# Performance work log

Measured on AMD Instinct MI355X. Metric: run time of the kernel, lower is better.

Reference implementation:

```python
import jax, jax.numpy as jnp
import numpy as np

B, T, E, H, L, Q, FF, V, C = 4, 2048, 16, 4, 2, 16, 64, 32000, 16
D = E // H  # head_dim = 4


def pos_encoding(t, e):
    # Sinusoidal PE, matching torch: pe[:,0::2]=sin, pe[:,1::2]=cos
    pos = jnp.arange(t, dtype=jnp.float32)[:, None]
    div = jnp.exp(jnp.arange(0, e, 2, dtype=jnp.float32) * (-np.log(10000.0) / e))
    ang = pos * div  # [T, E/2]
    return jnp.stack([jnp.sin(ang), jnp.cos(ang)], axis=-1).reshape(t, e)


def setup_inputs() -> dict:
    key = jax.random.key(0)
    ks = jax.random.split(key, 12)
    def n(k, shape, scale=0.1):
        return (jax.random.normal(k, shape) * scale).astype(jnp.float32)
    return {
        "tokens": jax.random.randint(ks[0], (B, T), 0, V),
        "emb": n(ks[1], (V, E)),
        "Wq": n(ks[2], (L, E, E)), "Wk": n(ks[3], (L, E, E)),
        "Wv": n(ks[4], (L, E, E)), "Wo": n(ks[5], (L, E, E)),
        "theta": n(ks[6], (L, Q), 1.0),
        "W1": n(ks[7], (L, E, FF)), "b1": jnp.zeros((L, FF), jnp.float32),
        "W2": n(ks[8], (L, FF, E)), "b2": jnp.zeros((L, E), jnp.float32),
        "gamma": jnp.ones((E,), jnp.float32), "beta": jnp.zeros((E,), jnp.float32),
        "Wc": n(ks[9], (E, C)), "bc": jnp.zeros((C,), jnp.float32),
    }


def reference(tokens, emb, Wq, Wk, Wv, Wo, theta, W1, b1, W2, b2, gamma, beta, Wc, bc):
    x = emb[tokens] + pos_encoding(T, E)[None]  # [B,T,E]
    for l in range(L):  # fixed small layer count
        # --- multi-head self-attention (no mask, eval mode: dropout off) ---
        q = (x @ Wq[l]).reshape(B, T, H, D)
        k = (x @ Wk[l]).reshape(B, T, H, D)
        v = (x @ Wv[l]).reshape(B, T, H, D)
        scores = jnp.einsum('bqhd,bkhd->bhqk', q, k) / np.sqrt(D).astype(np.float32)
        attn = jax.nn.softmax(scores, axis=-1)  # [B,H,T,T]
        o = jnp.einsum('bhqk,bkhd->bqhd', attn, v).reshape(B, T, E) @ Wo[l]
        x = x + o
        # --- quantum feed-forward ---
        # RX(x_w)|0> then RY(theta_w), measure PauliZ per wire. Single-qubit
        # gates on a product state factorize exactly: <Z_w> = cos(theta_w)*cos(x_w)
        q_out = jnp.cos(theta[l]) * jnp.cos(x)  # [B,T,E]
        h = jax.nn.relu(q_out @ W1[l] + b1[l])
        x = x + (h @ W2[l] + b2[l])
    # final LayerNorm
    mu = x.mean(-1, keepdims=True)
    var = ((x - mu) ** 2).mean(-1, keepdims=True)
    x = (x - mu) / jnp.sqrt(var + 1e-5) * gamma + beta
    # mean pool over tokens + classifier
    return x.mean(axis=1) @ Wc + bc  # [B,C]
```

## Files before the change

### kernel.cpp

```cpp
#include <hip/hip_runtime.h>
#include <hip/hip_bf16.h>
#include <math.h>

#define B_ 4
#define T_ 2048
#define E_ 16
#define H_ 4
#define D_ 4
#define L_ 2
#define FF_ 64
#define C_ 16

#define QSCALE 0.7213475204444817f

typedef __hip_bfloat16 bf16;
typedef _Float16 h8 __attribute__((ext_vector_type(8)));
typedef float f4 __attribute__((ext_vector_type(4)));

#if __has_builtin(__builtin_amdgcn_exp2f)
__device__ __forceinline__ float fast_exp2(float x) { return __builtin_amdgcn_exp2f(x); }
#else
__device__ __forceinline__ float fast_exp2(float x) { return exp2f(x); }
#endif

__device__ __forceinline__ unsigned short f2h(float f) {
  _Float16 h = (_Float16)f;
  return __builtin_bit_cast(unsigned short, h);
}
__device__ __forceinline__ _Float16 h2(unsigned short u) {
  return __builtin_bit_cast(_Float16, u);
}

__device__ __forceinline__ bool probe_bf16(const void* gamma) {
  return ((const unsigned*)gamma)[0] == 0x3F803F80u;
}
__device__ __forceinline__ float ldin(const void* p, int i, bool isb) {
  if (isb) {
    unsigned short u = ((const unsigned short*)p)[i];
    union { unsigned x; float f; } c; c.x = ((unsigned)u) << 16;
    return c.f;
  }
  return ((const float*)p)[i];
}
__device__ __forceinline__ void unpack2(unsigned u, float& a, float& b) {
  union { unsigned x; float f; } lo, hi;
  lo.x = u << 16; hi.x = u & 0xffff0000u;
  a = lo.f; b = hi.f;
}

__global__ __launch_bounds__(64) void embed_qkv_kernel(
    const int* __restrict__ tokens, const void* __restrict__ emb,
    const void* __restrict__ Wq, const void* __restrict__ Wk, const void* __restrict__ Wv,
    int wofs, const void* __restrict__ gamma,
    float* __restrict__ X, ushort4* __restrict__ Qhp, ushort4* __restrict__ Khp,
    float4* __restrict__ Vfp) {
  __shared__ float wq[256], wk[256], wv[256];
  bool isb = probe_bf16(gamma);
  int tid = threadIdx.x;
  #pragma unroll
  for (int i = tid; i < 256; i += 64) {
    wq[i] = ldin(Wq, wofs + i, isb);
    wk[i] = ldin(Wk, wofs + i, isb);
    wv[i] = ldin(Wv, wofs + i, isb);
  }
  int r = tid & 31, half = tid >> 5;
  int row = blockIdx.x * 32 + r;
  int t = row & (T_ - 1);
  int tok = tokens[row];
  float x[16];
  if (isb) {
    const unsigned short* eb = (const unsigned short*)emb + (size_t)tok * E_;
    uint4 e0 = ((const uint4*)eb)[0], e1 = ((const uint4*)eb)[1];
    unpack2(e0.x, x[0], x[1]);   unpack2(e0.y, x[2], x[3]);
    unpack2(e0.z, x[4], x[5]);   unpack2(e0.w, x[6], x[7]);
    unpack2(e1.x, x[8], x[9]);   unpack2(e1.y, x[10], x[11]);
    unpack2(e1.z, x[12], x[13]); unpack2(e1.w, x[14], x[15]);
  } else {
    const float* er = (const float*)emb + (size_t)tok * E_;
    #pragma unroll
    for (int i = 0; i < 4; i++) {
      float4 f = ((const float4*)er)[i];
      x[4*i+0] = f.x; x[4*i+1] = f.y; x[4*i+2] = f.z; x[4*i+3] = f.w;
    }
  }
  const float divs[8] = {1.f, 0.31622776601683794f, 0.1f, 0.031622776601683794f,
                         0.01f, 0.0031622776601683794f, 0.001f, 0.00031622776601683794f};
  #pragma unroll
  for (int i = 0; i < 8; i++) {
    float ang = (float)t * divs[i];
    x[2*i]   += __sinf(ang);
    x[2*i+1] += __cosf(ang);
  }
  __syncthreads();
  if (half == 0) {
    float* xr = X + (size_t)row * E_;
    #pragma unroll
    for (int i = 0; i < 4; i++)
      ((float4*)xr)[i] = make_float4(x[4*i], x[4*i+1], x[4*i+2], x[4*i+3]);
  }
  int b = row >> 11;
  #pragma unroll
  for (int hh = 0; hh < 2; hh++) {
    int h = half * 2 + hh;
    float q[4] = {0,0,0,0}, k[4] = {0,0,0,0}, v[4] = {0,0,0,0};
    #pragma unroll
    for (int e = 0; e < 16; e++) {
      float xv = x[e];
      #pragma unroll
      for (int d = 0; d < 4; d++) {
        q[d] = fmaf(xv, wq[e*16 + h*4 + d], q[d]);
        k[d] = fmaf(xv, wk[e*16 + h*4 + d], k[d]);
        v[d] = fmaf(xv, wv[e*16 + h*4 + d], v[d]);
      }
    }
    size_t idx = (size_t)(b * H_ + h) * T_ + t;
    Qhp[idx] = make_ushort4(f2h(q[0]*QSCALE), f2h(q[1]*QSCALE),
                            f2h(q[2]*QSCALE), f2h(q[3]*QSCALE));
    Khp[idx] = make_ushort4(f2h(k[0]), f2h(k[1]), f2h(k[2]), f2h(k[3]));
    Vfp[idx] = make_float4(v[0], v[1], v[2], v[3]);
  }
}

__global__ __launch_bounds__(256) void attn_kernel(
    const ushort4* __restrict__ Qhp, const ushort4* __restrict__ Khp,
    const float4* __restrict__ Vfp, float* __restrict__ Ob) {
  __shared__ float part[2][2][4][20];
  int blk = blockIdx.x;
  int bh = blk >> 6;
  int qp = blk & 63;
  int tid = threadIdx.x;
  int lane = tid & 63;
  int w = tid >> 6;
  int qt_l = w >> 1;
  int ks = w & 1;
  int qbase = qp * 32 + qt_l * 16;
  int kl = lane & 15;
  size_t bhT = (size_t)bh * T_;
  const _Float16 z = (_Float16)0.f;
  ushort4 qv = make_ushort4(0, 0, 0, 0);
  if (lane < 16) qv = Qhp[bhT + qbase + lane];
  h8 afrag = {h2(qv.x), h2(qv.y), h2(qv.z), h2(qv.w), z, z, z, z};
  f4 zero4 = {0.f, 0.f, 0.f, 0.f};
  float o[4][4] = {{0,0,0,0},{0,0,0,0},{0,0,0,0},{0,0,0,0}};
  float lr[4] = {0,0,0,0};
  int kt0 = ks * 64;
  #pragma unroll 4
  for (int kt = kt0; kt < kt0 + 64; kt++) {
    ushort4 kv = Khp[bhT + kt*16 + kl];
    if (lane >= 16) kv = make_ushort4(0, 0, 0, 0);
    h8 bfrag = {h2(kv.x), h2(kv.y), h2(kv.z), h2(kv.w), z, z, z, z};
    f4 sc = __builtin_amdgcn_mfma_f32_16x16x32_f16(afrag, bfrag, zero4, 0, 0, 0);
    float4 v = Vfp[bhT + kt*16 + kl];
    float p0 = fast_exp2(sc[0]), p1 = fast_exp2(sc[1]);
    float p2 = fast_exp2(sc[2]), p3 = fast_exp2(sc[3]);
    lr[0] += p0; lr[1] += p1; lr[2] += p2; lr[3] += p3;
    o[0][0] = fmaf(p0, v.x, o[0][0]); o[0][1] = fmaf(p0, v.y, o[0][1]);
    o[0][2] = fmaf(p0, v.z, o[0][2]); o[0][3] = fmaf(p0, v.w, o[0][3]);
    o[1][0] = fmaf(p1, v.x, o[1][0]); o[1][1] = fmaf(p1, v.y, o[1][1]);
    o[1][2] = fmaf(p1, v.z, o[1][2]); o[1][3] = fmaf(p1, v.w, o[1][3]);
    o[2][0] = fmaf(p2, v.x, o[2][0]); o[2][1] = fmaf(p2, v.y, o[2][1]);
    o[2][2] = fmaf(p2, v.z, o[2][2]); o[2][3] = fmaf(p2, v.w, o[2][3]);
    o[3][0] = fmaf(p3, v.x, o[3][0]); o[3][1] = fmaf(p3, v.y, o[3][1]);
    o[3][2] = fmaf(p3, v.z, o[3][2]); o[3][3] = fmaf(p3, v.w, o[3][3]);
  }
  #pragma unroll
  for (int m = 1; m < 16; m <<= 1) {
    #pragma unroll
    for (int r = 0; r < 4; r++) {
      lr[r] += __shfl_xor(lr[r], m, 64);
      #pragma unroll
      for (int d = 0; d < 4; d++) o[r][d] += __shfl_xor(o[r][d], m, 64);
    }
  }
  if ((lane & 15) == 0) {
    float* pp = &part[qt_l][ks][lane >> 4][0];
    #pragma unroll
    for (int r = 0; r < 4; r++) {
      #pragma unroll
      for (int d = 0; d < 4; d++) pp[r*4 + d] = o[r][d];
      pp[16 + r] = lr[r];
    }
  }
  __syncthreads();
  if (tid < 128) {
    int qt = tid >> 6, zz = tid & 63, q = zz >> 2, d = zz & 3;
    int g = q >> 2, r = q & 3;
    float ov = part[qt][0][g][r*4 + d] + part[qt][1][g][r*4 + d];
    float ls = part[qt][0][g][16 + r] + part[qt][1][g][16 + r];
    int b = bh >> 2, h = bh & 3;
    Ob[((size_t)b * T_ + qp*32 + qt*16 + q) * E_ + h*4 + d] = ov / ls;
  }
}

__global__ __launch_bounds__(64) void opff_qkv_kernel(
    const float* __restrict__ Ob, const void* __restrict__ Wo, int wofs,
    const void* __restrict__ theta, const void* __restrict__ W1, const void* __restrict__ b1,
    const void* __restrict__ W2, const void* __restrict__ b2, int l,
    const void* __restrict__ Wq, const void* __restrict__ Wk, const void* __restrict__ Wv,
    int wofs2, int do_qkv,
    const void* __restrict__ gamma, float* __restrict__ X,
    ushort4* __restrict__ Qhp, ushort4* __restrict__ Khp, float4* __restrict__ Vfp) {
  __shared__ float wo[256], w1[E_*FF_], w2[FF_*E_], s1[FF_], s2[E_], ct[E_];
  __shared__ float wq[256], wk[256], wv[256];
  bool isb = probe_bf16(gamma);
  int tid = threadIdx.x;
  int o1 = l * E_ * FF_;
  #pragma unroll
  for (int i = tid; i < 256; i += 64) wo[i] = ldin(Wo, wofs + i, isb);
  #pragma unroll
  for (int i = tid; i < E_*FF_; i += 64) {
    w1[i] = ldin(W1, o1 + i, isb);
    w2[i] = ldin(W2, o1 + i, isb);
  }
  if (tid < FF_) s1[tid] = ldin(b1, l*FF_ + tid, isb);
  if (tid < E_) {
    s2[tid] = ldin(b2, l*E_ + tid, isb);
    ct[tid] = cosf(ldin(theta, l*E_ + tid, isb));
  }
  if (do_qkv) {
    #pragma unroll
    for (int i = tid; i < 256; i += 64) {
      wq[i] = ldin(Wq, wofs2 + i, isb);
      wk[i] = ldin(Wk, wofs2 + i, isb);
      wv[i] = ldin(Wv, wofs2 + i, isb);
    }
  }
  __syncthreads();
  int r = tid & 31;
  int half = tid >> 5;
  size_t row = (size_t)blockIdx.x * 32 + r;
  float* xr = X + row * E_;
  const float* orow = Ob + row * E_;
  float x[16], o[16];
  #pragma unroll
  for (int i = 0; i < 4; i++) {
    float4 f = ((const float4*)xr)[i];
    x[4*i]=f.x; x[4*i+1]=f.y; x[4*i+2]=f.z; x[4*i+3]=f.w;
    float4 g = ((const float4*)orow)[i];
    o[4*i]=g.x; o[4*i+1]=g.y; o[4*i+2]=g.z; o[4*i+3]=g.w;
  }
  #pragma unroll
  for (int c = 0; c < 16; c++) {
    float s = 0.f;
    #pragma unroll
    for (int e = 0; e < 16; e++) s = fmaf(o[e], wo[e*16 + c], s);
    x[c] += s;
  }
  float qo[16];
  #pragma unroll
  for (int e = 0; e < 16; e++) qo[e] = ct[e] * __cosf(x[e]);
  float acc[16];
  #pragma unroll
  for (int e = 0; e < 16; e++) acc[e] = (half == 0) ? s2[e] : 0.f;
  int j0 = half * 32;
  for (int j = j0; j < j0 + 32; j++) {
    float s = s1[j];
    #pragma unroll
    for (int e = 0; e < 16; e++) s = fmaf(qo[e], w1[e*FF_ + j], s);
    s = fmaxf(s, 0.f);
    #pragma unroll
    for (int e = 0; e < 16; e++) acc[e] = fmaf(s, w2[j*E_ + e], acc[e]);
  }
  #pragma unroll
  for (int e = 0; e < 16; e++) acc[e] += __shfl_xor(acc[e], 32, 64);
  #pragma unroll
  for (int e = 0; e < 16; e++) x[e] += acc[e];
  if (half == 0) {
    #pragma unroll
    for (int i = 0; i < 4; i++)
      ((float4*)xr)[i] = make_float4(x[4*i], x[4*i+1], x[4*i+2], x[4*i+3]);
  }
  if (do_qkv) {
    int b = (int)(row >> 11), t = (int)(row & (T_ - 1));
    #pragma unroll
    for (int hh = 0; hh < 2; hh++) {
      int h = half * 2 + hh;
      float q[4] = {0,0,0,0}, k[4] = {0,0,0,0}, v[4] = {0,0,0,0};
      #pragma unroll
      for (int e = 0; e < 16; e++) {
        float xv = x[e];
        #pragma unroll
        for (int d = 0; d < 4; d++) {
          q[d] = fmaf(xv, wq[e*16 + h*4 + d], q[d]);
          k[d] = fmaf(xv, wk[e*16 + h*4 + d], k[d]);
          v[d] = fmaf(xv, wv[e*16 + h*4 + d], v[d]);
        }
      }
      size_t idx = (size_t)(b * H_ + h) * T_ + t;
      Qhp[idx] = make_ushort4(f2h(q[0]*QSCALE), f2h(q[1]*QSCALE),
                              f2h(q[2]*QSCALE), f2h(q[3]*QSCALE));
      Khp[idx] = make_ushort4(f2h(k[0]), f2h(k[1]), f2h(k[2]), f2h(k[3]));
      Vfp[idx] = make_float4(v[0], v[1], v[2], v[3]);
    }
  }
}

__global__ __launch_bounds__(1024) void lnfin_kernel(
    const float* __restrict__ X, const void* __restrict__ gamma,
    const void* __restrict__ beta, const void* __restrict__ Wc,
    const void* __restrict__ bc, float* __restrict__ out) {
  __shared__ float sg[16], sb[16], wsum[16][16], pool[16];
  bool isb = probe_bf16(gamma);
  int tid = threadIdx.x;
  int b = blockIdx.x;
  if (tid < 16) { sg[tid] = ldin(gamma, tid, isb); sb[tid] = ldin(beta, tid, isb); }
  __syncthreads();
  float acc[16];
  #pragma unroll
  for (int e = 0; e < 16; e++) acc[e] = 0.f;
  #pragma unroll
  for (int rr = 0; rr < 2; rr++) {
    int r = tid + rr * 1024;
    const float* xr = X + ((size_t)b * T_ + r) * E_;
    float x[16];
    #pragma unroll
    for (int i = 0; i < 4; i++) {
      float4 f = ((const float4*)xr)[i];
      x[4*i]=f.x; x[4*i+1]=f.y; x[4*i+2]=f.z; x[4*i+3]=f.w;
    }
    float mu = 0.f;
    #pragma unroll
    for (int e = 0; e < 16; e++) mu += x[e];
    mu *= (1.f/16.f);
    float var = 0.f;
    #pragma unroll
    for (int e = 0; e < 16; e++) { float d = x[e]-mu; var = fmaf(d, d, var); }
    var *= (1.f/16.f);
    float inv = rsqrtf(var + 1e-5f);
    #pragma unroll
    for (int e = 0; e < 16; e++) acc[e] += (x[e]-mu)*inv*sg[e] + sb[e];
  }
  #pragma unroll
  for (int e = 0; e < 16; e++) {
    float s = acc[e];
    #pragma unroll
    for (int m = 1; m < 64; m <<= 1) s += __shfl_xor(s, m, 64);
    acc[e] = s;
  }
  int wid = tid >> 6;
  if ((tid & 63) == 0) {
    #pragma unroll
    for (int e = 0; e < 16; e++) wsum[wid][e] = acc[e];
  }
  __syncthreads();
  if (tid < 16) {
    float s = 0.f;
    #pragma unroll
    for (int w = 0; w < 16; w++) s += wsum[w][tid];
    pool[tid] = s * (1.f / T_);
  }
  __syncthreads();
  if (tid < 16) {
    float a = ldin(bc, tid, isb);
    #pragma unroll
    for (int e = 0; e < 16; e++) a = fmaf(pool[e], ldin(Wc, e*16 + tid, isb), a);
    out[b * 16 + tid] = a;
  }
}

extern "C" void kernel_launch(void* const* d_in, const int* in_sizes, int n_in,
                              void* d_out, int out_size, void* d_ws, size_t ws_size,
                              hipStream_t stream) {
  const int*  tokens = (const int*)d_in[0];
  const void* emb    = d_in[1];
  const void* Wq     = d_in[2];
  const void* Wk     = d_in[3];
  const void* Wv     = d_in[4];
  const void* Wo     = d_in[5];
  const void* theta  = d_in[6];
  const void* W1     = d_in[7];
  const void* b1     = d_in[8];
  const void* W2     = d_in[9];
  const void* b2     = d_in[10];
  const void* gamma  = d_in[11];
  const void* beta   = d_in[12];
  const void* Wc     = d_in[13];
  const void* bc     = d_in[14];

  float* ws = (float*)d_ws;
  float*   X   = ws;
  ushort4* Qhp = (ushort4*)(ws + 131072);
  ushort4* Khp = (ushort4*)(ws + 196608);
  float4*  Vfp = (float4*)(ws + 262144);
  float*   Ob  = ws + 393216;
  float* out = (float*)d_out;

  embed_qkv_kernel<<<256, 64, 0, stream>>>(tokens, emb, Wq, Wk, Wv, 0, gamma,
                                           X, Qhp, Khp, Vfp);
  for (int l = 0; l < L_; l++) {
    attn_kernel<<<16*64, 256, 0, stream>>>(Qhp, Khp, Vfp, Ob);
    int wofs = l * E_ * E_;
    int wofs2 = (l + 1) * E_ * E_;
    int do_qkv = (l + 1 < L_) ? 1 : 0;
    opff_qkv_kernel<<<256, 64, 0, stream>>>(Ob, Wo, wofs, theta, W1, b1, W2, b2, l,
                                            Wq, Wk, Wv, wofs2, do_qkv,
                                            gamma, X, Qhp, Khp, Vfp);
  }
  lnfin_kernel<<<B_, 1024, 0, stream>>>(X, gamma, beta, Wc, bc, out);
}
```

Measured before the change: 95.43 us.

## Compute attention P·V with a second MFMA using a transposed fp16 V layout

The attention loop now computes S^T so that the exponentiated scores sit in the B-operand layout of a 16x16x16 f16 MFMA. A second MFMA then accumulates V^T·P, with an extra row of ones that yields the softmax row sums. A new transposed fp16 V buffer is written by the QKV producers to feed this. The change replaces 16 scalar FMAs per tile and the cross-lane shuffle reduction. In exchange it adds an fp16 rounding of the probabilities and V, and an extra global write of V.

```diff
diff --git a/kernel.cpp b/kernel.cpp
--- a/kernel.cpp
+++ b/kernel.cpp
@@ -15,7 +15,14 @@
 
 typedef __hip_bfloat16 bf16;
 typedef _Float16 h8 __attribute__((ext_vector_type(8)));
+typedef _Float16 h4 __attribute__((ext_vector_type(4)));
 typedef float f4 __attribute__((ext_vector_type(4)));
+
+#if __has_builtin(__builtin_amdgcn_mfma_f32_16x16x16f16)
+#define HAVE_MFMA16 1
+#else
+#define HAVE_MFMA16 0
+#endif
 
 #if __has_builtin(__builtin_amdgcn_exp2f)
 __device__ __forceinline__ float fast_exp2(float x) { return __builtin_amdgcn_exp2f(x); }
@@ -53,7 +60,7 @@
     const void* __restrict__ Wq, const void* __restrict__ Wk, const void* __restrict__ Wv,
     int wofs, const void* __restrict__ gamma,
     float* __restrict__ X, ushort4* __restrict__ Qhp, ushort4* __restrict__ Khp,
-    float4* __restrict__ Vfp) {
+    unsigned short* __restrict__ Vth, float4* __restrict__ Vfp) {
   __shared__ float wq[256], wk[256], wv[256];
   bool isb = probe_bf16(gamma);
   int tid = threadIdx.x;
@@ -113,18 +120,23 @@
         v[d] = fmaf(xv, wv[e*16 + h*4 + d], v[d]);
       }
     }
-    size_t idx = (size_t)(b * H_ + h) * T_ + t;
+    size_t bh = (size_t)(b * H_ + h);
+    size_t idx = bh * T_ + t;
     Qhp[idx] = make_ushort4(f2h(q[0]*QSCALE), f2h(q[1]*QSCALE),
                             f2h(q[2]*QSCALE), f2h(q[3]*QSCALE));
     Khp[idx] = make_ushort4(f2h(k[0]), f2h(k[1]), f2h(k[2]), f2h(k[3]));
+    #pragma unroll
+    for (int d = 0; d < 4; d++) Vth[(bh * 4 + d) * T_ + t] = f2h(v[d]);
     Vfp[idx] = make_float4(v[0], v[1], v[2], v[3]);
   }
 }
 
 __global__ __launch_bounds__(256) void attn_kernel(
     const ushort4* __restrict__ Qhp, const ushort4* __restrict__ Khp,
-    const float4* __restrict__ Vfp, float* __restrict__ Ob) {
-  __shared__ float part[2][2][4][20];
+    const unsigned short* __restrict__ Vth, const float4* __restrict__ Vfp,
+    float* __restrict__ Ob) {
+  __shared__ float pnum[2][2][16][4];
+  __shared__ float pl2[2][2][16];
   int blk = blockIdx.x;
   int bh = blk >> 6;
   int qp = blk & 63;
@@ -134,61 +146,83 @@
   int qt_l = w >> 1;
   int ks = w & 1;
   int qbase = qp * 32 + qt_l * 16;
-  int kl = lane & 15;
   size_t bhT = (size_t)bh * T_;
   const _Float16 z = (_Float16)0.f;
   ushort4 qv = make_ushort4(0, 0, 0, 0);
   if (lane < 16) qv = Qhp[bhT + qbase + lane];
-  h8 afrag = {h2(qv.x), h2(qv.y), h2(qv.z), h2(qv.w), z, z, z, z};
+  h8 bq = {h2(qv.x), h2(qv.y), h2(qv.z), h2(qv.w), z, z, z, z};
   f4 zero4 = {0.f, 0.f, 0.f, 0.f};
-  float o[4][4] = {{0,0,0,0},{0,0,0,0},{0,0,0,0},{0,0,0,0}};
-  float lr[4] = {0,0,0,0};
+  int g = lane >> 4;
+  int dl = lane & 15;
   int kt0 = ks * 64;
+#if HAVE_MFMA16
+  const unsigned short* vbase = Vth + (size_t)bh * 4 * T_;
+  f4 oacc = {0.f, 0.f, 0.f, 0.f};
   #pragma unroll 4
   for (int kt = kt0; kt < kt0 + 64; kt++) {
-    ushort4 kv = Khp[bhT + kt*16 + kl];
-    if (lane >= 16) kv = make_ushort4(0, 0, 0, 0);
-    h8 bfrag = {h2(kv.x), h2(kv.y), h2(kv.z), h2(kv.w), z, z, z, z};
-    f4 sc = __builtin_amdgcn_mfma_f32_16x16x32_f16(afrag, bfrag, zero4, 0, 0, 0);
-    float4 v = Vfp[bhT + kt*16 + kl];
-    float p0 = fast_exp2(sc[0]), p1 = fast_exp2(sc[1]);
-    float p2 = fast_exp2(sc[2]), p3 = fast_exp2(sc[3]);
-    lr[0] += p0; lr[1] += p1; lr[2] += p2; lr[3] += p3;
-    o[0][0] = fmaf(p0, v.x, o[0][0]); o[0][1] = fmaf(p0, v.y, o[0][1]);
-    o[0][2] = fmaf(p0, v.z, o[0][2]); o[0][3] = fmaf(p0, v.w, o[0][3]);
-    o[1][0] = fmaf(p1, v.x, o[1][0]); o[1][1] = fmaf(p1, v.y, o[1][1]);
-    o[1][2] = fmaf(p1, v.z, o[1][2]); o[1][3] = fmaf(p1, v.w, o[1][3]);
-    o[2][0] = fmaf(p2, v.x, o[2][0]); o[2][1] = fmaf(p2, v.y, o[2][1]);
-    o[2][2] = fmaf(p2, v.z, o[2][2]); o[2][3] = fmaf(p2, v.w, o[2][3]);
-    o[3][0] = fmaf(p3, v.x, o[3][0]); o[3][1] = fmaf(p3, v.y, o[3][1]);
-    o[3][2] = fmaf(p3, v.z, o[3][2]); o[3][3] = fmaf(p3, v.w, o[3][3]);
-  }
-  #pragma unroll
-  for (int m = 1; m < 16; m <<= 1) {
+    ushort4 kv = make_ushort4(0, 0, 0, 0);
+    if (lane < 16) kv = Khp[bhT + kt*16 + lane];
+    h8 ak = {h2(kv.x), h2(kv.y), h2(kv.z), h2(kv.w), z, z, z, z};
+    f4 st = __builtin_amdgcn_mfma_f32_16x16x32_f16(ak, bq, zero4, 0, 0, 0);
+    h4 pb = {(_Float16)fast_exp2(st[0]), (_Float16)fast_exp2(st[1]),
+             (_Float16)fast_exp2(st[2]), (_Float16)fast_exp2(st[3])};
+    h4 a2;
+    if (dl < 4) {
+      ushort4 vv = *(const ushort4*)(vbase + (size_t)dl * T_ + kt*16 + 4*g);
+      a2 = (h4){h2(vv.x), h2(vv.y), h2(vv.z), h2(vv.w)};
+    } else if (dl == 4) {
+      a2 = (h4){(_Float16)1.f, (_Float16)1.f, (_Float16)1.f, (_Float16)1.f};
+    } else {
+      a2 = (h4){z, z, z, z};
+    }
+    oacc = __builtin_amdgcn_mfma_f32_16x16x16f16(a2, pb, oacc, 0, 0, 0);
+  }
+  float lval = __shfl(oacc[0], 16 + dl, 64);
+  if (lane < 16) {
+    pnum[qt_l][ks][lane][0] = oacc[0];
+    pnum[qt_l][ks][lane][1] = oacc[1];
+    pnum[qt_l][ks][lane][2] = oacc[2];
+    pnum[qt_l][ks][lane][3] = oacc[3];
+    pl2[qt_l][ks][lane] = lval;
+  }
+#else
+  (void)Vth;
+  float num[4] = {0,0,0,0};
+  float lsum = 0.f;
+  #pragma unroll 4
+  for (int kt = kt0; kt < kt0 + 64; kt++) {
+    ushort4 kv = make_ushort4(0, 0, 0, 0);
+    if (lane < 16) kv = Khp[bhT + kt*16 + lane];
+    h8 ak = {h2(kv.x), h2(kv.y), h2(kv.z), h2(kv.w), z, z, z, z};
+    f4 st = __builtin_amdgcn_mfma_f32_16x16x32_f16(ak, bq, zero4, 0, 0, 0);
     #pragma unroll
     for (int r = 0; r < 4; r++) {
-      lr[r] += __shfl_xor(lr[r], m, 64);
-      #pragma unroll
-      for (int d = 0; d < 4; d++) o[r][d] += __shfl_xor(o[r][d], m, 64);
-    }
-  }
-  if ((lane & 15) == 0) {
-    float* pp = &part[qt_l][ks][lane >> 4][0];
-    #pragma unroll
-    for (int r = 0; r < 4; r++) {
-      #pragma unroll
-      for (int d = 0; d < 4; d++) pp[r*4 + d] = o[r][d];
-      pp[16 + r] = lr[r];
-    }
-  }
+      float p = fast_exp2(st[r]);
+      lsum += p;
+      float4 v = Vfp[bhT + kt*16 + 4*g + r];
+      num[0] = fmaf(p, v.x, num[0]); num[1] = fmaf(p, v.y, num[1]);
+      num[2] = fmaf(p, v.z, num[2]); num[3] = fmaf(p, v.w, num[3]);
+    }
+  }
+  #pragma unroll
+  for (int m = 16; m < 64; m <<= 1) {
+    lsum += __shfl_xor(lsum, m, 64);
+    #pragma unroll
+    for (int d = 0; d < 4; d++) num[d] += __shfl_xor(num[d], m, 64);
+  }
+  if (lane < 16) {
+    #pragma unroll
+    for (int d = 0; d < 4; d++) pnum[qt_l][ks][lane][d] = num[d];
+    pl2[qt_l][ks][lane] = lsum;
+  }
+#endif
   __syncthreads();
   if (tid < 128) {
-    int qt = tid >> 6, zz = tid & 63, q = zz >> 2, d = zz & 3;
-    int g = q >> 2, r = q & 3;
-    float ov = part[qt][0][g][r*4 + d] + part[qt][1][g][r*4 + d];
-    float ls = part[qt][0][g][16 + r] + part[qt][1][g][16 + r];
+    int qt = tid >> 6, rest = tid & 63, q = rest >> 2, d = rest & 3;
+    float nv = pnum[qt][0][q][d] + pnum[qt][1][q][d];
+    float lv = pl2[qt][0][q] + pl2[qt][1][q];
     int b = bh >> 2, h = bh & 3;
-    Ob[((size_t)b * T_ + qp*32 + qt*16 + q) * E_ + h*4 + d] = ov / ls;
+    Ob[((size_t)b * T_ + qp*32 + qt*16 + q) * E_ + h*4 + d] = nv / lv;
   }
 }
 
@@ -199,7 +233,8 @@
     const void* __restrict__ Wq, const void* __restrict__ Wk, const void* __restrict__ Wv,
     int wofs2, int do_qkv,
     const void* __restrict__ gamma, float* __restrict__ X,
-    ushort4* __restrict__ Qhp, ushort4* __restrict__ Khp, float4* __restrict__ Vfp) {
+    ushort4* __restrict__ Qhp, ushort4* __restrict__ Khp,
+    unsigned short* __restrict__ Vth, float4* __restrict__ Vfp) {
   __shared__ float wo[256], w1[E_*FF_], w2[FF_*E_], s1[FF_], s2[E_], ct[E_];
   __shared__ float wq[256], wk[256], wv[256];
   bool isb = probe_bf16(gamma);
@@ -286,10 +321,13 @@
           v[d] = fmaf(xv, wv[e*16 + h*4 + d], v[d]);
         }
       }
-      size_t idx = (size_t)(b * H_ + h) * T_ + t;
+      size_t bh = (size_t)(b * H_ + h);
+      size_t idx = bh * T_ + t;
       Qhp[idx] = make_ushort4(f2h(q[0]*QSCALE), f2h(q[1]*QSCALE),
                               f2h(q[2]*QSCALE), f2h(q[3]*QSCALE));
       Khp[idx] = make_ushort4(f2h(k[0]), f2h(k[1]), f2h(k[2]), f2h(k[3]));
+      #pragma unroll
+      for (int d = 0; d < 4; d++) Vth[(bh * 4 + d) * T_ + t] = f2h(v[d]);
       Vfp[idx] = make_float4(v[0], v[1], v[2], v[3]);
     }
   }
@@ -378,23 +416,24 @@
   const void* bc     = d_in[14];
 
   float* ws = (float*)d_ws;
-  float*   X   = ws;
-  ushort4* Qhp = (ushort4*)(ws + 131072);
-  ushort4* Khp = (ushort4*)(ws + 196608);
-  float4*  Vfp = (float4*)(ws + 262144);
-  float*   Ob  = ws + 393216;
+  float*          X   = ws;
+  ushort4*        Qhp = (ushort4*)(ws + 131072);
+  ushort4*        Khp = (ushort4*)(ws + 196608);
+  unsigned short* Vth = (unsigned short*)(ws + 262144);
+  float4*         Vfp = (float4*)(ws + 327680);
+  float*          Ob  = ws + 458752;
   float* out = (float*)d_out;
 
   embed_qkv_kernel<<<256, 64, 0, stream>>>(tokens, emb, Wq, Wk, Wv, 0, gamma,
-                                           X, Qhp, Khp, Vfp);
+                                           X, Qhp, Khp, Vth, Vfp);
   for (int l = 0; l < L_; l++) {
-    attn_kernel<<<16*64, 256, 0, stream>>>(Qhp, Khp, Vfp, Ob);
+    attn_kernel<<<16*64, 256, 0, stream>>>(Qhp, Khp, Vth, Vfp, Ob);
     int wofs = l * E_ * E_;
     int wofs2 = (l + 1) * E_ * E_;
     int do_qkv = (l + 1 < L_) ? 1 : 0;
     opff_qkv_kernel<<<256, 64, 0, stream>>>(Ob, Wo, wofs, theta, W1, b1, W2, b2, l,
                                             Wq, Wk, Wv, wofs2, do_qkv,
-                                            gamma, X, Qhp, Khp, Vfp);
+                                            gamma, X, Qhp, Khp, Vth, Vfp);
   }
   lnfin_kernel<<<B_, 1024, 0, stream>>>(X, gamma, beta, Wc, bc, out);
 }
```

New measurement: 107.8 us. 1.13x slower.
